# Kernel optimization log

Measured on AMD Instinct MI355X. Metric: run time of the kernel, lower is better.

## Reference

```python
import jax, jax.numpy as jnp
import numpy as np

B = 16384
STATE = 524   # state_dim / output_size
IENC = 256    # INet output dim
ZD = 32       # z_dim
H = 256       # expert hidden size
E = 5         # num_experts
HG = 256      # gating hidden size
IN1 = STATE + IENC + ZD   # 812, PredictionNet layer-1 input
IN2 = H + ZD              # 288, layers 2/3 input


def _uni(k, shape):
    # matches PredictionNet.init_params glorot-style uniform bound
    bound = float(np.sqrt(6.0 / (shape[-2] * shape[-1])))
    return jax.random.uniform(k, shape, jnp.float32, -bound, bound)


def setup_inputs() -> dict:
    key = jax.random.key(0)
    ks = jax.random.split(key, 12)
    d = {}
    d['z'] = jax.random.normal(ks[0], (B, ZD), jnp.float32)
    d['p_prev'] = jax.random.normal(ks[1], (B, STATE), jnp.float32)
    d['I'] = jax.random.normal(ks[2], (B, 2048), jnp.float32)
    # gating network: (state+z) -> HG -> HG//2 -> E
    d['gw1'] = _uni(ks[3], (STATE + ZD, HG)); d['gb1'] = jnp.zeros((HG,), jnp.float32)
    d['gw2'] = _uni(ks[4], (HG, HG // 2));    d['gb2'] = jnp.zeros((HG // 2,), jnp.float32)
    d['gw3'] = _uni(ks[5], (HG // 2, E));     d['gb3'] = jnp.zeros((E,), jnp.float32)
    # INet: 2048 -> 256 -> 256 -> 256
    d['iw1'] = _uni(ks[6], (2048, IENC)); d['ib1'] = jnp.zeros((IENC,), jnp.float32)
    d['iw2'] = _uni(ks[7], (IENC, IENC)); d['ib2'] = jnp.zeros((IENC,), jnp.float32)
    d['iw3'] = _uni(ks[8], (IENC, IENC)); d['ib3'] = jnp.zeros((IENC,), jnp.float32)
    # expert weights [E, in, out], biases [E, out]
    d['w_l1'] = _uni(ks[9], (E, IN1, H));     d['b_l1'] = jnp.zeros((E, H), jnp.float32)
    d['w_l2'] = _uni(ks[10], (E, IN2, H));    d['b_l2'] = jnp.zeros((E, H), jnp.float32)
    d['w_l3'] = _uni(ks[11], (E, IN2, STATE)); d['b_l3'] = jnp.zeros((E, STATE), jnp.float32)
    return d


def reference(z, p_prev, I, gw1, gb1, gw2, gb2, gw3, gb3,
              iw1, ib1, iw2, ib2, iw3, ib3,
              w_l1, b_l1, w_l2, b_l2, w_l3, b_l3):
    elu = jax.nn.elu
    # gating network -> softmax blending coefficients omega [B, E]
    g = elu(jnp.concatenate([z, p_prev], axis=1) @ gw1 + gb1)
    g = elu(g @ gw2 + gb2)
    omega = jax.nn.softmax(g @ gw3 + gb3, axis=-1)
    # interaction encoder
    Ienc = elu(elu(elu(I @ iw1 + ib1) @ iw2 + ib2) @ iw3 + ib3)
    x = jnp.concatenate([p_prev, Ienc], axis=1)  # [B, STATE+IENC]

    def moe_linear(h, W, b):
        # same math as sum_e omega_e * (h @ W_e) + omega @ b, without
        # materializing per-sample blended [B, in, out] weights
        per_expert = jnp.einsum('bi,eio->beo', h, W)
        return jnp.einsum('be,beo->bo', omega, per_expert) + omega @ b

    h0 = jnp.concatenate([z, x], axis=1)          # [B, 812]
    h1 = elu(moe_linear(h0, w_l1, b_l1))          # [B, 256]
    h2 = elu(moe_linear(jnp.concatenate([z, h1], axis=1), w_l2, b_l2))
    h3 = moe_linear(jnp.concatenate([z, h2], axis=1), w_l3, b_l3)  # [B, 524]
    return h3
```

## Files before the change

kernel.cpp:

```cpp
#include <hip/hip_runtime.h>
#include <hip/hip_bf16.h>
#include <cstdint>
#include <cstddef>


#define BATCH 16384

typedef __attribute__((ext_vector_type(8))) short short8;
typedef __attribute__((ext_vector_type(4))) float f32x4;
typedef unsigned short u16;
typedef unsigned int u32;

typedef __attribute__((address_space(3))) void lds_t;
typedef __attribute__((address_space(1))) void gmem_t;

__device__ __forceinline__ void gload16(const u16* g, u16* l) {
  __builtin_amdgcn_global_load_lds((gmem_t*)(u16*)g, (lds_t*)l, 16, 0, 0);
}

__device__ __forceinline__ void barrier_nodrain() {
  asm volatile("" ::: "memory");
  __builtin_amdgcn_s_barrier();
  asm volatile("" ::: "memory");
}
__device__ __forceinline__ void barrier_lds() {
  asm volatile("s_waitcnt lgkmcnt(0)" ::: "memory");
  __builtin_amdgcn_s_barrier();
  asm volatile("" ::: "memory");
}

__device__ __forceinline__ float bf2f(u16 u) {
  union { float f; u32 i; } v; v.i = ((u32)u) << 16; return v.f;
}
__device__ __forceinline__ u16 f2bf(float f) {
  union { float f; u32 i; } v; v.f = f;
  u32 x = v.i;
  return (u16)((x + 0x7fffu + ((x >> 16) & 1u)) >> 16);
}
__device__ __forceinline__ u16 load_bf(const void* p, long i, int f32) {
  return f32 ? f2bf(((const float*)p)[i]) : ((const u16*)p)[i];
}
__device__ __forceinline__ float elu_f(float x) { return x > 0.f ? x : expm1f(x); }

__device__ __forceinline__ int swz(int row, int q) { return q ^ ((row >> 1) & 3); }

struct TPSeg { long end; int K, N, Kp, Np; };

__global__ __launch_bounds__(256) void prep_all(
    const void* __restrict__ z, const void* __restrict__ p,
    const void* __restrict__ I, int* __restrict__ flagp,
    u16* __restrict__ h0, u16* __restrict__ h1c, u16* __restrict__ h2c,
    u16* __restrict__ Ibf,
    const void* ib1, const void* ib2, const void* ib3,
    const void* gb1, const void* gb2, const void* gb3,
    const void* gw3, const void* bl1, const void* bl2, const void* bl3,
    u16* __restrict__ smallc,
    const void* s0, const void* s1, const void* s2, const void* s3,
    const void* s4, const void* s5, const void* s6, const void* s7,
    u16* d0, u16* d1, u16* d2, u16* d3, u16* d4, u16* d5, u16* d6, u16* d7)
{
  __shared__ int scnt[4];
  {
    u32 w = ((const u32*)z)[threadIdx.x];
    int e = (w >> 7) & 0xFF;
    unsigned long long m = __ballot(e >= 112 && e <= 142);
    if ((threadIdx.x & 63) == 0) scnt[threadIdx.x >> 6] = __popcll(m);
  }
  __syncthreads();
  const int f32 = (scnt[0] + scnt[1] + scnt[2] + scnt[3] < 128) ? 1 : 0;
  if (blockIdx.x == 0 && threadIdx.x == 0) *flagp = f32;

  if (blockIdx.x == 0) {
    for (long j = threadIdx.x; j < 7100; j += 256) {
      u16 v;
      if      (j < 256)  v = load_bf(ib1, j,        f32);
      else if (j < 512)  v = load_bf(ib2, j - 256,  f32);
      else if (j < 768)  v = load_bf(ib3, j - 512,  f32);
      else if (j < 1024) v = load_bf(gb1, j - 768,  f32);
      else if (j < 1152) v = load_bf(gb2, j - 1024, f32);
      else if (j < 1280) v = (j - 1152 < 5) ? load_bf(gb3, j - 1152, f32) : (u16)0;
      else if (j < 1920) v = load_bf(gw3, j - 1280, f32);
      else if (j < 3200) v = load_bf(bl1, j - 1920, f32);
      else if (j < 4480) v = load_bf(bl2, j - 3200, f32);
      else               v = load_bf(bl3, j - 4480, f32);
      smallc[j] = v;
    }
  }

  const TPSeg seg[8] = {
    {  524288, 2048, 256, 2048, 256 },
    {  589824,  256, 256,  256, 256 },
    {  655360,  256, 256,  256, 256 },
    {  802816,  556, 256,  576, 256 },
    {  835584,  256, 128,  256, 128 },
    { 1900544,  812, 256,  832, 256 },
    { 2269184,  288, 256,  288, 256 },
    { 3098624,  288, 524,  288, 576 },
  };
  const void* const srcs[8] = { s0, s1, s2, s3, s4, s5, s6, s7 };
  u16* const dsts[8] = { d0, d1, d2, d3, d4, d5, d6, d7 };

  const long NC = (long)BATCH * 2048 / 8;
  const long NP = (long)BATCH * 104;
  const long NT = 3098624 / 4;
  const long total = NC + NP + NT;
  const long stride = (long)gridDim.x * blockDim.x;

  for (long it = (long)blockIdx.x * 256 + threadIdx.x; it < total; it += stride) {
    if (it < NC) {
      if (f32) {
        const long t = it;
        const float4* src = (const float4*)I;
        float4 a = src[t * 2], b = src[t * 2 + 1];
        union { u16 r[8]; uint4 v; } u;
        u.r[0] = f2bf(a.x); u.r[1] = f2bf(a.y); u.r[2] = f2bf(a.z); u.r[3] = f2bf(a.w);
        u.r[4] = f2bf(b.x); u.r[5] = f2bf(b.y); u.r[6] = f2bf(b.z); u.r[7] = f2bf(b.w);
        *(uint4*)(Ibf + t * 8) = u.v;
      }
    } else if (it < NC + NP) {
      const long j = it - NC;
      const int b = (int)(j / 104);
      const int c = (int)(j % 104) * 8;
      uint4 w; w.x = 0; w.y = 0; w.z = 0; w.w = 0;
      if (c < 32) {
        if (f32) {
          const float4 f0 = *(const float4*)((const float*)z + (long)b * 32 + c);
          const float4 f1 = *(const float4*)((const float*)z + (long)b * 32 + c + 4);
          w.x = (u32)f2bf(f0.x) | ((u32)f2bf(f0.y) << 16);
          w.y = (u32)f2bf(f0.z) | ((u32)f2bf(f0.w) << 16);
          w.z = (u32)f2bf(f1.x) | ((u32)f2bf(f1.y) << 16);
          w.w = (u32)f2bf(f1.z) | ((u32)f2bf(f1.w) << 16);
        } else {
          w = *(const uint4*)((const u16*)z + (long)b * 32 + c);
        }
        *(uint4*)(h0 + (long)b * 832 + c) = w;
        *(uint4*)(h1c + (long)b * 288 + c) = w;
        *(uint4*)(h2c + (long)b * 288 + c) = w;
        continue;
      }
      if (c < 552) {
        const long pi = (long)b * 524 + (c - 32);
        if (f32) {
          const float4 f0 = *(const float4*)((const float*)p + pi);
          const float4 f1 = *(const float4*)((const float*)p + pi + 4);
          w.x = (u32)f2bf(f0.x) | ((u32)f2bf(f0.y) << 16);
          w.y = (u32)f2bf(f0.z) | ((u32)f2bf(f0.w) << 16);
          w.z = (u32)f2bf(f1.x) | ((u32)f2bf(f1.y) << 16);
          w.w = (u32)f2bf(f1.z) | ((u32)f2bf(f1.w) << 16);
        } else {
          const uint2 a0 = *(const uint2*)((const u16*)p + pi);
          const uint2 a1 = *(const uint2*)((const u16*)p + pi + 4);
          w.x = a0.x; w.y = a0.y; w.z = a1.x; w.w = a1.y;
        }
      } else if (c == 552) {
        const long pi = (long)b * 524 + 520;
        if (f32) {
          const float4 f0 = *(const float4*)((const float*)p + pi);
          w.x = (u32)f2bf(f0.x) | ((u32)f2bf(f0.y) << 16);
          w.y = (u32)f2bf(f0.z) | ((u32)f2bf(f0.w) << 16);
        } else {
          const uint2 a0 = *(const uint2*)((const u16*)p + pi);
          w.x = a0.x; w.y = a0.y;
        }
      }
      *(uint4*)(h0 + (long)b * 832 + c) = w;
    } else {
      const long jd = (it - NC - NP) * 4;
      int s = 0; long sbase = 0;
      while (jd >= seg[s].end) { sbase = seg[s].end; ++s; }
      const long jj = jd - sbase;
      const int Kp = seg[s].Kp, Np = seg[s].Np, Kk = seg[s].K, Nn = seg[s].N;
      const int k = (int)(jj % Kp);
      const long tt = jj / Kp;
      const int n = (int)(tt % Np);
      const int e = (int)(tt / Np);
      ushort4 v; v.x = 0; v.y = 0; v.z = 0; v.w = 0;
      if (k < Kk && n < Nn) {
        const long sb = (long)e * Kk * Nn + (long)k * Nn + n;
        v.x = load_bf(srcs[s], sb, f32);
        v.y = load_bf(srcs[s], sb + Nn, f32);
        v.z = load_bf(srcs[s], sb + 2 * (long)Nn, f32);
        v.w = load_bf(srcs[s], sb + 3 * (long)Nn, f32);
      }
      *(ushort4*)(dsts[s] + jj) = v;
    }
  }
}

struct GemmDesc {
  const u16* A; const u16* Aalt; const u16* Wt; const u16* bias; u16* C;
  int lda, ldw, ldc, col_off, K, ny, a_mode;
};

__global__ __launch_bounds__(256, 4) void gemm64m(GemmDesc da, GemmDesc db,
                                                  const int* __restrict__ flagp)
{
  __shared__ __align__(16) u16 sA[3][64 * 32];
  __shared__ __align__(16) u16 sB[3][128 * 32];

  int bn = blockIdx.y;
  GemmDesc d;
  if (bn < da.ny) { d = da; } else { bn -= da.ny; d = db; }
  const u16* Abase = (d.a_mode && *flagp) ? d.Aalt : d.A;

  const int tid  = threadIdx.x;
  const int bm   = blockIdx.x;
  const int lane = tid & 63, wave = tid >> 6;
  const int wm = (wave & 1) * 32, wn = (wave >> 1) * 64;
  const int lrow = lane & 15, lq = lane >> 4;

  const int sq    = (lane & 3) ^ ((lane >> 3) & 3);
  const int srowA = 16 * wave + (lane >> 2);
  const int srowB = 32 * wave + (lane >> 2);
  const u16* Ag = Abase + (size_t)(bm * 64  + srowA) * d.lda + sq * 8;
  const u16* Wg = d.Wt  + (size_t)(bn * 128 + srowB) * d.ldw + sq * 8;
  const int laOff = wave * 512;
  const int lbOff = wave * 1024;
  const int ldw = d.ldw;

  f32x4 acc[2][4] = {};
  const int nt = d.K / 32;

  gload16(Ag, sA[0] + laOff);
  gload16(Wg, sB[0] + lbOff);
  gload16(Wg + (size_t)16 * ldw, sB[0] + lbOff + 512);
  gload16(Ag + 32, sA[1] + laOff);
  gload16(Wg + 32, sB[1] + lbOff);
  gload16(Wg + (size_t)16 * ldw + 32, sB[1] + lbOff + 512);

  for (int t = 0; t < nt; ++t) {
    const int cur = t % 3;
    barrier_nodrain();
    if (t + 2 < nt) {
      const int nb = (t + 2) % 3;
      const int k0 = (t + 2) * 32;
      gload16(Ag + k0, sA[nb] + laOff);
      gload16(Wg + k0, sB[nb] + lbOff);
      gload16(Wg + (size_t)16 * ldw + k0, sB[nb] + lbOff + 512);
    }
    const int ahead = nt - 1 - t;
    if (ahead >= 2)      asm volatile("s_waitcnt vmcnt(6)" ::: "memory");
    else if (ahead == 1) asm volatile("s_waitcnt vmcnt(3)" ::: "memory");
    else                 asm volatile("s_waitcnt vmcnt(0)" ::: "memory");
    barrier_nodrain();

    short8 a[2], b[4];
#pragma unroll
    for (int i = 0; i < 2; ++i) {
      const int r = wm + i * 16 + lrow;
      a[i] = *(const short8*)(sA[cur] + r * 32 + swz(r, lq) * 8);
    }
#pragma unroll
    for (int i = 0; i < 4; ++i) {
      const int r = wn + i * 16 + lrow;
      b[i] = *(const short8*)(sB[cur] + r * 32 + swz(r, lq) * 8);
    }

    __builtin_amdgcn_s_setprio(1);
#pragma unroll
    for (int mi = 0; mi < 2; ++mi)
#pragma unroll
      for (int ni = 0; ni < 4; ++ni)
        acc[mi][ni] = __builtin_amdgcn_mfma_f32_16x16x32_bf16(a[mi], b[ni], acc[mi][ni], 0, 0, 0);
    __builtin_amdgcn_s_setprio(0);
  }

#pragma unroll
  for (int ni = 0; ni < 4; ++ni) {
    const int col = bn * 128 + wn + ni * 16 + lrow;
    const float bv = bf2f(d.bias[col]);
#pragma unroll
    for (int mi = 0; mi < 2; ++mi) {
#pragma unroll
      for (int r = 0; r < 4; ++r) {
        const int row = bm * 64 + wm + mi * 16 + lq * 4 + r;
        float v = acc[mi][ni][r] + bv;
        v = elu_f(v);
        d.C[(size_t)row * d.ldc + d.col_off + col] = f2bf(v);
      }
    }
  }
}

template<bool ELU>
__global__ __launch_bounds__(256, 2) void moe_gemm(
    const u16* __restrict__ A, int lda,
    const u16* __restrict__ Wt, int ldw, long wstride_e,
    const u16* __restrict__ bias, int bias_n,
    const u16* __restrict__ g2, const u16* __restrict__ gw3c,
    const u16* __restrict__ gb3c,
    void* __restrict__ C, int ldc, int col_off, int n_store, int K,
    const int* __restrict__ flagp, int is_final)
{
  __shared__ __align__(16) u16 sA[2][128 * 32];
  __shared__ __align__(16) u16 sW[2][5 * 64 * 32];
  __shared__ float som[128 * 5];
  __shared__ float sbias[5][64];
  __shared__ float sgw[128 * 5];
  __shared__ float sgb[5];

  const int tid  = threadIdx.x;
  const int bm   = blockIdx.x, bn = blockIdx.y;
  const int lane = tid & 63, wave = tid >> 6;
  const int wm = (wave & 1) * 64, wn = (wave >> 1) * 32;
  const int lrow = lane & 15, lq = lane >> 4;
  const int f32out = is_final ? *flagp : 0;

  const int sq = (lane & 3) ^ ((lane >> 3) & 3);
  const int srowA = 32 * wave + (lane >> 2);
  const int srowW = 16 * wave + (lane >> 2);
  const u16* Ag = A  + (size_t)(bm * 128 + srowA) * lda + sq * 8;
  const u16* Wg = Wt + (size_t)(bn * 64 + srowW) * ldw + sq * 8;
  const int laOff = wave * 1024;
  const int lWoff = wave * 512;

  auto stage = [&](int buf, int k0) {
    gload16(Ag + k0, sA[buf] + laOff);
    gload16(Ag + (size_t)16 * lda + k0, sA[buf] + laOff + 512);
#pragma unroll
    for (int e = 0; e < 5; ++e)
      gload16(Wg + e * wstride_e + k0, sW[buf] + e * 2048 + lWoff);
  };

  f32x4 acc[5][4][2] = {};
  const int nt = K / 32;

  stage(0, 0);
  for (int t2 = tid; t2 < 960; t2 += 256) {
    if (t2 < 640) {
      sgw[t2] = bf2f(gw3c[t2]);
    } else {
      const int j = t2 - 640;
      const int e = j >> 6, c = j & 63;
      const int col = bn * 64 + c;
      sbias[e][c] = (col < bias_n) ? bf2f(bias[(size_t)e * bias_n + col]) : 0.f;
    }
  }
  if (tid < 5) sgb[tid] = bf2f(gb3c[tid]);
  barrier_lds();
  if (tid < 128) {
    const u16* gr = g2 + (size_t)(bm * 128 + tid) * 128;
    float t[5];
#pragma unroll
    for (int e = 0; e < 5; ++e) t[e] = sgb[e];
    for (int k = 0; k < 128; k += 2) {
      const u32 gp = *(const u32*)(gr + k);
      const float x0 = bf2f((u16)(gp & 0xffffu));
      const float x1 = bf2f((u16)(gp >> 16));
#pragma unroll
      for (int e = 0; e < 5; ++e)
        t[e] += x0 * sgw[k * 5 + e] + x1 * sgw[(k + 1) * 5 + e];
    }
    float m = t[0];
#pragma unroll
    for (int e = 1; e < 5; ++e) m = fmaxf(m, t[e]);
    float ssum = 0.f;
#pragma unroll
    for (int e = 0; e < 5; ++e) { t[e] = expf(t[e] - m); ssum += t[e]; }
    const float inv = 1.f / ssum;
#pragma unroll
    for (int e = 0; e < 5; ++e) som[tid * 5 + e] = t[e] * inv;
  }

  for (int t = 0; t < nt; ++t) {
    const int cur = t & 1;
    barrier_nodrain();
    if (t + 1 < nt) {
      stage(cur ^ 1, (t + 1) * 32);
      asm volatile("s_waitcnt vmcnt(7)" ::: "memory");
    } else {
      asm volatile("s_waitcnt vmcnt(0)" ::: "memory");
    }
    barrier_nodrain();

    short8 a[4];
#pragma unroll
    for (int i = 0; i < 4; ++i) {
      const int r = wm + i * 16 + lrow;
      a[i] = *(const short8*)(sA[cur] + r * 32 + swz(r, lq) * 8);
    }
    const int rb0 = wn + lrow, rb1 = rb0 + 16;
    const int ob0 = rb0 * 32 + swz(rb0, lq) * 8;
    const int ob1 = rb1 * 32 + swz(rb1, lq) * 8;
    __builtin_amdgcn_s_setprio(1);
#pragma unroll
    for (int e = 0; e < 5; ++e) {
      short8 b0 = *(const short8*)(sW[cur] + e * 2048 + ob0);
      short8 b1 = *(const short8*)(sW[cur] + e * 2048 + ob1);
#pragma unroll
      for (int mi = 0; mi < 4; ++mi) {
        acc[e][mi][0] = __builtin_amdgcn_mfma_f32_16x16x32_bf16(a[mi], b0, acc[e][mi][0], 0, 0, 0);
        acc[e][mi][1] = __builtin_amdgcn_mfma_f32_16x16x32_bf16(a[mi], b1, acc[e][mi][1], 0, 0, 0);
      }
    }
    __builtin_amdgcn_s_setprio(0);
  }

#pragma unroll
  for (int mi = 0; mi < 4; ++mi) {
#pragma unroll
    for (int r = 0; r < 4; ++r) {
      const int rl = wm + mi * 16 + lq * 4 + r;
      const int row = bm * 128 + rl;
      float om[5];
#pragma unroll
      for (int e = 0; e < 5; ++e) om[e] = som[rl * 5 + e];
#pragma unroll
      for (int ni = 0; ni < 2; ++ni) {
        const int c = wn + ni * 16 + lrow;
        const int col = bn * 64 + c;
        if (col < n_store) {
          float v = 0.f;
#pragma unroll
          for (int e = 0; e < 5; ++e) v += om[e] * (acc[e][mi][ni][r] + sbias[e][c]);
          if (ELU) v = elu_f(v);
          const size_t idx = (size_t)row * ldc + col_off + col;
          if (f32out) ((float*)C)[idx] = v;
          else        ((u16*)C)[idx]   = f2bf(v);
        }
      }
    }
  }
}

extern "C" void kernel_launch(void* const* d_in, const int* in_sizes, int n_in,
                              void* d_out, int out_size, void* d_ws, size_t ws_size,
                              hipStream_t stream)
{
  const void* z    = d_in[0];
  const void* pprev= d_in[1];
  const void* I    = d_in[2];
  const void* gw1  = d_in[3];
  const void* gb1  = d_in[4];
  const void* gw2  = d_in[5];
  const void* gb2  = d_in[6];
  const void* gw3  = d_in[7];
  const void* gb3  = d_in[8];
  const void* iw1  = d_in[9];
  const void* ib1  = d_in[10];
  const void* iw2  = d_in[11];
  const void* ib2  = d_in[12];
  const void* iw3  = d_in[13];
  const void* ib3  = d_in[14];
  const void* wl1  = d_in[15];
  const void* bl1  = d_in[16];
  const void* wl2  = d_in[17];
  const void* bl2  = d_in[18];
  const void* wl3  = d_in[19];
  const void* bl3  = d_in[20];

  char* base = (char*)d_ws;
  size_t off = 0;
  auto alloc = [&](size_t bytes) -> void* {
    void* p = base + off;
    off = (off + bytes + 255) & ~(size_t)255;
    return p;
  };

  const size_t B = BATCH;
  int* flagp   = (int*)alloc(256);
  u16* h0      = (u16*)alloc(B * 832 * 2);
  u16* h1c     = (u16*)alloc(B * 288 * 2);
  u16* h2c     = (u16*)alloc(B * 288 * 2);
  u16* i1      = (u16*)alloc(B * 256 * 2);
  u16* i2      = (u16*)alloc(B * 256 * 2);
  u16* g1      = (u16*)alloc(B * 256 * 2);
  u16* g2      = (u16*)alloc(B * 128 * 2);
  u16* Ibf     = (u16*)alloc(B * 2048 * 2);
  u16* smallc  = (u16*)alloc(7100 * 2);
  u16* iw1t = (u16*)alloc((size_t)256 * 2048 * 2);
  u16* iw2t = (u16*)alloc((size_t)256 * 256 * 2);
  u16* iw3t = (u16*)alloc((size_t)256 * 256 * 2);
  u16* gw1t = (u16*)alloc((size_t)256 * 576 * 2);
  u16* gw2t = (u16*)alloc((size_t)128 * 256 * 2);
  u16* wl1t = (u16*)alloc((size_t)5 * 256 * 832 * 2);
  u16* wl2t = (u16*)alloc((size_t)5 * 256 * 288 * 2);
  u16* wl3t = (u16*)alloc((size_t)5 * 576 * 288 * 2);
  (void)in_sizes; (void)n_in; (void)out_size; (void)ws_size;

  u16* ib1c = smallc + 0,   *ib2c = smallc + 256, *ib3c = smallc + 512;
  u16* gb1c = smallc + 768, *gb2c = smallc + 1024, *gb3c = smallc + 1152;
  u16* gw3c = smallc + 1280;
  u16* bl1c = smallc + 1920, *bl2c = smallc + 3200, *bl3c = smallc + 4480;

  prep_all<<<2048, 256, 0, stream>>>(z, pprev, I, flagp, h0, h1c, h2c, Ibf,
      ib1, ib2, ib3, gb1, gb2, gb3, gw3, bl1, bl2, bl3, smallc,
      iw1, iw2, iw3, gw1, gw2, wl1, wl2, wl3,
      iw1t, iw2t, iw3t, gw1t, gw2t, wl1t, wl2t, wl3t);

  GemmDesc inet1 = { (const u16*)I, Ibf, iw1t, ib1c, i1, 2048, 2048, 256, 0,   2048, 2, 1 };
  GemmDesc gat1  = { h0, h0, gw1t, gb1c, g1,  832,  576, 256, 0,    576, 2, 0 };
  GemmDesc inet2 = { i1, i1, iw2t, ib2c, i2,  256,  256, 256, 0,    256, 2, 0 };
  GemmDesc gat2  = { g1, g1, gw2t, gb2c, g2,  256,  256, 128, 0,    256, 1, 0 };
  GemmDesc inet3 = { i2, i2, iw3t, ib3c, h0,  256,  256, 832, 556,  256, 2, 0 };

  gemm64m<<<dim3(BATCH/64, 4), 256, 0, stream>>>(inet1, gat1, flagp);
  gemm64m<<<dim3(BATCH/64, 3), 256, 0, stream>>>(inet2, gat2, flagp);
  gemm64m<<<dim3(BATCH/64, 2), 256, 0, stream>>>(inet3, inet3, flagp);

  moe_gemm<true><<<dim3(BATCH/128, 4), 256, 0, stream>>>(
      h0, 832, wl1t, 832, (long)256 * 832, bl1c, 256, g2, gw3c, gb3c,
      h1c, 288, 32, 256, 832, flagp, 0);
  moe_gemm<true><<<dim3(BATCH/128, 4), 256, 0, stream>>>(
      h1c, 288, wl2t, 288, (long)256 * 288, bl2c, 256, g2, gw3c, gb3c,
      h2c, 288, 32, 256, 288, flagp, 0);
  moe_gemm<false><<<dim3(BATCH/128, 9), 256, 0, stream>>>(
      h2c, 288, wl3t, 288, (long)576 * 288, bl3c, 524, g2, gw3c, gb3c,
      d_out, 524, 0, 524, 288, flagp, 1);
}
```

Measured before the change: 517.1 us.

## Transpose weights through per-wave LDS tiles and split prep loops by phase

Replaces the per-element strided weight transpose, which used a segment search and uncoalesced column reads, with per-wave 32x32 tiles staged in padded shared memory. Reads and writes become row-contiguous vector accesses. The single fused grid-stride loop is also split into separate loops for the I conversion (now 16 elements per thread), the h0 packing and the weight transpose. This removes per-iteration branching. The cost is extra LDS traffic, and the transpose relies on wave-synchronous LDS use with no barrier between the tile write and the tile read.

```diff
diff --git a/kernel.cpp b/kernel.cpp
--- a/kernel.cpp
+++ b/kernel.cpp
@@ -43,8 +43,6 @@
 __device__ __forceinline__ float elu_f(float x) { return x > 0.f ? x : expm1f(x); }
 
 __device__ __forceinline__ int swz(int row, int q) { return q ^ ((row >> 1) & 3); }
-
-struct TPSeg { long end; int K, N, Kp, Np; };
 
 __global__ __launch_bounds__(256) void prep_all(
     const void* __restrict__ z, const void* __restrict__ p,
@@ -60,6 +58,7 @@
     u16* d0, u16* d1, u16* d2, u16* d3, u16* d4, u16* d5, u16* d6, u16* d7)
 {
   __shared__ int scnt[4];
+  __shared__ u16 tl[4][32][33];
   {
     u32 w = ((const u32*)z)[threadIdx.x];
     int e = (w >> 7) & 0xFF;
@@ -87,40 +86,33 @@
     }
   }
 
-  const TPSeg seg[8] = {
-    {  524288, 2048, 256, 2048, 256 },
-    {  589824,  256, 256,  256, 256 },
-    {  655360,  256, 256,  256, 256 },
-    {  802816,  556, 256,  576, 256 },
-    {  835584,  256, 128,  256, 128 },
-    { 1900544,  812, 256,  832, 256 },
-    { 2269184,  288, 256,  288, 256 },
-    { 3098624,  288, 524,  288, 576 },
-  };
-  const void* const srcs[8] = { s0, s1, s2, s3, s4, s5, s6, s7 };
-  u16* const dsts[8] = { d0, d1, d2, d3, d4, d5, d6, d7 };
-
-  const long NC = (long)BATCH * 2048 / 8;
-  const long NP = (long)BATCH * 104;
-  const long NT = 3098624 / 4;
-  const long total = NC + NP + NT;
-  const long stride = (long)gridDim.x * blockDim.x;
-
-  for (long it = (long)blockIdx.x * 256 + threadIdx.x; it < total; it += stride) {
-    if (it < NC) {
-      if (f32) {
-        const long t = it;
-        const float4* src = (const float4*)I;
-        float4 a = src[t * 2], b = src[t * 2 + 1];
-        union { u16 r[8]; uint4 v; } u;
-        u.r[0] = f2bf(a.x); u.r[1] = f2bf(a.y); u.r[2] = f2bf(a.z); u.r[3] = f2bf(a.w);
-        u.r[4] = f2bf(b.x); u.r[5] = f2bf(b.y); u.r[6] = f2bf(b.z); u.r[7] = f2bf(b.w);
-        *(uint4*)(Ibf + t * 8) = u.v;
-      }
-    } else if (it < NC + NP) {
-      const long j = it - NC;
-      const int b = (int)(j / 104);
-      const int c = (int)(j % 104) * 8;
+  const long gid = (long)blockIdx.x * 256 + threadIdx.x;
+  const long stride = (long)gridDim.x * 256;
+
+  if (f32) {
+    const long NCt = (long)BATCH * 2048 / 16;
+    for (long it = gid; it < NCt; it += stride) {
+      const float4* sI = (const float4*)I + it * 4;
+      const float4 a = sI[0], b = sI[1], c4 = sI[2], d4 = sI[3];
+      uint4 w0, w1;
+      w0.x = (u32)f2bf(a.x)  | ((u32)f2bf(a.y)  << 16);
+      w0.y = (u32)f2bf(a.z)  | ((u32)f2bf(a.w)  << 16);
+      w0.z = (u32)f2bf(b.x)  | ((u32)f2bf(b.y)  << 16);
+      w0.w = (u32)f2bf(b.z)  | ((u32)f2bf(b.w)  << 16);
+      w1.x = (u32)f2bf(c4.x) | ((u32)f2bf(c4.y) << 16);
+      w1.y = (u32)f2bf(c4.z) | ((u32)f2bf(c4.w) << 16);
+      w1.z = (u32)f2bf(d4.x) | ((u32)f2bf(d4.y) << 16);
+      w1.w = (u32)f2bf(d4.z) | ((u32)f2bf(d4.w) << 16);
+      *(uint4*)(Ibf + it * 16)     = w0;
+      *(uint4*)(Ibf + it * 16 + 8) = w1;
+    }
+  }
+
+  {
+    const long NP = (long)BATCH * 104;
+    for (long it = gid; it < NP; it += stride) {
+      const int b = (int)(it / 104);
+      const int c = (int)(it % 104) * 8;
       uint4 w; w.x = 0; w.y = 0; w.z = 0; w.w = 0;
       if (c < 32) {
         if (f32) {
@@ -164,25 +156,78 @@
         }
       }
       *(uint4*)(h0 + (long)b * 832 + c) = w;
-    } else {
-      const long jd = (it - NC - NP) * 4;
-      int s = 0; long sbase = 0;
-      while (jd >= seg[s].end) { sbase = seg[s].end; ++s; }
-      const long jj = jd - sbase;
-      const int Kp = seg[s].Kp, Np = seg[s].Np, Kk = seg[s].K, Nn = seg[s].N;
-      const int k = (int)(jj % Kp);
-      const long tt = jj / Kp;
-      const int n = (int)(tt % Np);
-      const int e = (int)(tt / Np);
-      ushort4 v; v.x = 0; v.y = 0; v.z = 0; v.w = 0;
-      if (k < Kk && n < Nn) {
-        const long sb = (long)e * Kk * Nn + (long)k * Nn + n;
-        v.x = load_bf(srcs[s], sb, f32);
-        v.y = load_bf(srcs[s], sb + Nn, f32);
-        v.z = load_bf(srcs[s], sb + 2 * (long)Nn, f32);
-        v.w = load_bf(srcs[s], sb + 3 * (long)Nn, f32);
-      }
-      *(ushort4*)(dsts[s] + jj) = v;
+    }
+  }
+
+  {
+    const void* const srcs[8] = { s0, s1, s2, s3, s4, s5, s6, s7 };
+    u16* const dsts[8] = { d0, d1, d2, d3, d4, d5, d6, d7 };
+    const int tKp[8] = { 2048, 256, 256, 576, 256, 832, 288, 288 };
+    const int tNp[8] = {  256, 256, 256, 256, 128, 256, 256, 576 };
+    const int tK [8] = { 2048, 256, 256, 556, 256, 812, 288, 288 };
+    const int tN [8] = {  256, 256, 256, 256, 128, 256, 256, 524 };
+    const int wave = threadIdx.x >> 6, lane = threadIdx.x & 63;
+    const int rl = lane >> 3;
+    const int cl = (lane & 7) * 4;
+
+    for (int t = blockIdx.x * 4 + wave; t < 3026; t += gridDim.x * 4) {
+      int s, base;
+      if      (t < 512)  { s = 0; base = 0; }
+      else if (t < 576)  { s = 1; base = 512; }
+      else if (t < 640)  { s = 2; base = 576; }
+      else if (t < 784)  { s = 3; base = 640; }
+      else if (t < 816)  { s = 4; base = 784; }
+      else if (t < 1856) { s = 5; base = 816; }
+      else if (t < 2216) { s = 6; base = 1856; }
+      else               { s = 7; base = 2216; }
+      const int tt = t - base;
+      const int Kp = tKp[s], Np = tNp[s], K = tK[s], N = tN[s];
+      const int Ktl = Kp >> 5;
+      const int kt  = tt % Ktl;
+      const int r2  = tt / Ktl;
+      const int ntb = r2 % (Np >> 5);
+      const int e   = r2 / (Np >> 5);
+      const void* src = srcs[s];
+      u16* dst = dsts[s];
+      const long ebase = (long)e * K * N;
+
+#pragma unroll
+      for (int j = 0; j < 4; ++j) {
+        const int kr = kt * 32 + rl + 8 * j;
+        const int nc = ntb * 32 + cl;
+        ushort4 v; v.x = 0; v.y = 0; v.z = 0; v.w = 0;
+        if (kr < K) {
+          const long sb = ebase + (long)kr * N + nc;
+          if (nc + 3 < N) {
+            if (f32) {
+              const float4 f = *(const float4*)((const float*)src + sb);
+              v.x = f2bf(f.x); v.y = f2bf(f.y); v.z = f2bf(f.z); v.w = f2bf(f.w);
+            } else {
+              v = *(const ushort4*)((const u16*)src + sb);
+            }
+          } else {
+            if (nc     < N) v.x = load_bf(src, sb,     f32);
+            if (nc + 1 < N) v.y = load_bf(src, sb + 1, f32);
+            if (nc + 2 < N) v.z = load_bf(src, sb + 2, f32);
+            if (nc + 3 < N) v.w = load_bf(src, sb + 3, f32);
+          }
+        }
+        tl[wave][rl + 8 * j][cl + 0] = v.x;
+        tl[wave][rl + 8 * j][cl + 1] = v.y;
+        tl[wave][rl + 8 * j][cl + 2] = v.z;
+        tl[wave][rl + 8 * j][cl + 3] = v.w;
+      }
+#pragma unroll
+      for (int j = 0; j < 4; ++j) {
+        const int nr = ntb * 32 + rl + 8 * j;
+        const int kc = kt * 32 + cl;
+        ushort4 v;
+        v.x = tl[wave][cl + 0][rl + 8 * j];
+        v.y = tl[wave][cl + 1][rl + 8 * j];
+        v.z = tl[wave][cl + 2][rl + 8 * j];
+        v.w = tl[wave][cl + 3][rl + 8 * j];
+        *(ushort4*)(dst + (long)e * Np * Kp + (long)nr * Kp + kc) = v;
+      }
     }
   }
 }
```

Result: no change. 509.4 us (-1.5%).
